# Performance work log

Hardware: AMD Instinct MI355X
Metric: run time of the kernel (lower is better)

## Reference

```python
import jax, jax.numpy as jnp
import numpy as np

DIM = 768
NUM_HEADS = 12
HEAD_DIM = 64  # attn_head_dim override
ALL_HEAD_DIM = NUM_HEADS * HEAD_DIM  # 768
SCALE = HEAD_DIM ** -0.5


def setup_inputs() -> dict:
    key = jax.random.key(0)
    ks = jax.random.split(key, 6)
    B, N = 8, 1024
    x = jax.random.normal(ks[0], (B, N, DIM), dtype=jnp.float32)
    w_qkv = jax.random.normal(ks[1], (3 * ALL_HEAD_DIM, DIM), dtype=jnp.float32) * (DIM ** -0.5)
    q_bias = jnp.zeros((ALL_HEAD_DIM,), dtype=jnp.float32)
    v_bias = jnp.zeros((ALL_HEAD_DIM,), dtype=jnp.float32)
    w_proj = jax.random.normal(ks[2], (DIM, ALL_HEAD_DIM), dtype=jnp.float32) * (ALL_HEAD_DIM ** -0.5)
    b_proj = jnp.zeros((DIM,), dtype=jnp.float32)
    return {"x": x, "w_qkv": w_qkv, "q_bias": q_bias, "v_bias": v_bias,
            "w_proj": w_proj, "b_proj": b_proj}


def reference(x, w_qkv, q_bias, v_bias, w_proj, b_proj):
    B, N, C = x.shape
    # qkv bias: [q_bias, zeros (k has no bias), v_bias]
    qkv_bias = jnp.concatenate([q_bias, jnp.zeros_like(v_bias), v_bias])
    qkv = x @ w_qkv.T + qkv_bias                      # [B, N, 3*ALL_HEAD_DIM]
    qkv = qkv.reshape(B, N, 3, NUM_HEADS, HEAD_DIM).transpose(2, 0, 3, 1, 4)
    q, k, v = qkv[0], qkv[1], qkv[2]                  # each [B, H, N, D]
    attn = jnp.einsum('bhqd,bhkd->bhqk', q * SCALE, k)
    attn = jax.nn.softmax(attn, axis=-1)
    out = jnp.einsum('bhqk,bhkd->bhqd', attn, v)      # [B, H, N, D]
    out = out.transpose(0, 2, 1, 3).reshape(B, N, ALL_HEAD_DIM)
    out = out @ w_proj.T + b_proj                     # [B, N, C]
    return out
```

## Files before the change

kernel.cpp:

```cpp
#include <hip/hip_runtime.h>
#include <hip/hip_bf16.h>

typedef unsigned short u16;
typedef unsigned int u32;
typedef __attribute__((ext_vector_type(4))) float f32x4;
typedef __attribute__((ext_vector_type(16))) float f32x16;
typedef __attribute__((ext_vector_type(8))) short bf16x8;

__device__ inline u16 f2bf(float f) {
    union { float f; u32 u; } v; v.f = f;
    u32 r = v.u + 0x7fff + ((v.u >> 16) & 1);
    return (u16)(r >> 16);
}

__device__ inline f32x4 mfma16(bf16x8 a, bf16x8 b, f32x4 c) {
    return __builtin_amdgcn_mfma_f32_16x16x32_bf16(a, b, c, 0, 0, 0);
}
__device__ inline f32x16 mfma32(bf16x8 a, bf16x8 b, f32x16 c) {
    return __builtin_amdgcn_mfma_f32_32x32x16_bf16(a, b, c, 0, 0, 0);
}
__device__ inline u32 cvtpk(float lo, float hi) {
    u32 r;
    asm("v_cvt_pk_bf16_f32 %0, %1, %2" : "=v"(r) : "v"(lo), "v"(hi));
    return r;
}
__device__ inline float exp2v(float x) {
    float r;
    asm("v_exp_f32 %0, %1" : "=v"(r) : "v"(x));
    return r;
}

__device__ inline void gload_lds16(const void* g, const void* l) {
    __builtin_amdgcn_global_load_lds(
        (const __attribute__((address_space(1))) void*)g,
        (__attribute__((address_space(3))) void*)l, 16, 0, 0);
}

#define QSCALE 0.18033688f

__global__ void cvt_kernel(const float* __restrict__ in, u16* __restrict__ out, int n8) {
    int i = blockIdx.x * 256 + threadIdx.x;
    if (i >= n8) return;
    const float4* p = (const float4*)in;
    float4 a = p[2 * i], b = p[2 * i + 1];
    bf16x8 v;
    v[0] = (short)f2bf(a.x); v[1] = (short)f2bf(a.y);
    v[2] = (short)f2bf(a.z); v[3] = (short)f2bf(a.w);
    v[4] = (short)f2bf(b.x); v[5] = (short)f2bf(b.y);
    v[6] = (short)f2bf(b.z); v[7] = (short)f2bf(b.w);
    ((bf16x8*)out)[i] = v;
}

template <int EPI>
__global__ __launch_bounds__(256) void gemm_bt(
    const u16* __restrict__ A, const u16* __restrict__ B,
    int M, int N, int K,
    u16* __restrict__ qw, u16* __restrict__ kw, u16* __restrict__ vw,
    const float* __restrict__ qb, const float* __restrict__ vb,
    float* __restrict__ outp, const float* __restrict__ bproj)
{
    __shared__ __align__(16) u16 lA[2][128 * 32];
    __shared__ __align__(16) u16 lB[2][128 * 32];
    const int tid = threadIdx.x;
    const int lane = tid & 63;
    const int wv = tid >> 6;
    const int nbn = N >> 7;
    const int bm = blockIdx.x / nbn, bn = blockIdx.x % nbn;
    const int row0 = bm << 7, col0 = bn << 7;

    const int c0 = tid, c1 = tid + 256;
    const int ldsOff0 = (wv * 64) * 8;
    const int ldsOff1 = (256 + wv * 64) * 8;

    f32x4 acc[4][4];
#pragma unroll
    for (int i = 0; i < 4; i++)
#pragma unroll
        for (int j = 0; j < 4; j++) acc[i][j] = (f32x4){0.f, 0.f, 0.f, 0.f};

    const int nT = K >> 5;

    auto stage = [&](int buf, int t) {
        const int k0 = t << 5;
        gload_lds16(&A[(size_t)(row0 + (c0 >> 2)) * K + k0 + (c0 & 3) * 8], &lA[buf][ldsOff0]);
        gload_lds16(&A[(size_t)(row0 + (c1 >> 2)) * K + k0 + (c1 & 3) * 8], &lA[buf][ldsOff1]);
        gload_lds16(&B[(size_t)(col0 + (c0 >> 2)) * K + k0 + (c0 & 3) * 8], &lB[buf][ldsOff0]);
        gload_lds16(&B[(size_t)(col0 + (c1 >> 2)) * K + k0 + (c1 & 3) * 8], &lB[buf][ldsOff1]);
    };

    const int wr = (wv >> 1) << 6;
    const int wc = (wv & 1) << 6;

    stage(0, 0);
    __syncthreads();
    for (int t = 0; t < nT; ++t) {
        if (t + 1 < nT) stage((t + 1) & 1, t + 1);
        const int buf = t & 1;
        const u16* As = &lA[buf][(wr + (lane & 15)) * 32 + ((lane >> 4) * 8)];
        const u16* Bs = &lB[buf][(wc + (lane & 15)) * 32 + ((lane >> 4) * 8)];
        bf16x8 af[4], bfr[4];
#pragma unroll
        for (int i = 0; i < 4; i++) af[i] = *(const bf16x8*)(As + i * 16 * 32);
#pragma unroll
        for (int i = 0; i < 4; i++) bfr[i] = *(const bf16x8*)(Bs + i * 16 * 32);
#pragma unroll
        for (int i = 0; i < 4; i++)
#pragma unroll
            for (int j = 0; j < 4; j++)
                acc[i][j] = mfma16(af[i], bfr[j], acc[i][j]);
        __syncthreads();
    }

    if (EPI == 0) {
#pragma unroll
        for (int nj = 0; nj < 4; ++nj) {
            const int col = col0 + wc + nj * 16 + (lane & 15);
            const int part = col / 768;
            const int rem = col - part * 768;
            const int h = rem >> 6, d = rem & 63;
            if (part == 2) {
                const float bias = vb[rem];
                const int fbase = ((d >> 5) << 1);
                const int dl = d & 31;
#pragma unroll
                for (int mi = 0; mi < 4; ++mi) {
                    const int rowb = row0 + wr + mi * 16 + ((lane >> 4) << 2);
                    const int bb = rowb >> 10, nb = rowb & 1023;
                    const int t2 = nb >> 5, kin = nb & 31;
                    const int f = fbase + (kin >> 4);
                    const int lane_ = (((kin >> 3) & 1) << 5) + dl;
                    ushort4 pk;
                    pk.x = f2bf(acc[mi][nj][0] + bias);
                    pk.y = f2bf(acc[mi][nj][1] + bias);
                    pk.z = f2bf(acc[mi][nj][2] + bias);
                    pk.w = f2bf(acc[mi][nj][3] + bias);
                    *(ushort4*)&vw[((size_t)(bb * 12 + h) << 16) + (t2 << 11) +
                                   (f << 9) + (lane_ << 3) + (nb & 7)] = pk;
                }
            } else if (part == 1) {
                const int joff = (d >> 3) << 8, e = d & 7;
#pragma unroll
                for (int mi = 0; mi < 4; ++mi) {
#pragma unroll
                    for (int j = 0; j < 4; ++j) {
                        const int row = row0 + wr + mi * 16 + ((lane >> 4) << 2) + j;
                        const int bb = row >> 10, n = row & 1023;
                        kw[((size_t)(bb * 12 + h) << 16) + ((n >> 5) << 11) + joff +
                           ((n & 31) << 3) + e] = f2bf(acc[mi][nj][j]);
                    }
                }
            } else {
                const float bias = qb[rem];
#pragma unroll
                for (int mi = 0; mi < 4; ++mi) {
#pragma unroll
                    for (int j = 0; j < 4; ++j) {
                        const int row = row0 + wr + mi * 16 + ((lane >> 4) << 2) + j;
                        const int bb = row >> 10, n = row & 1023;
                        qw[(size_t)(((bb * 12 + h) << 10) + n) * 64 + d] =
                            f2bf((acc[mi][nj][j] + bias) * QSCALE);
                    }
                }
            }
        }
    } else {
#pragma unroll
        for (int nj = 0; nj < 4; ++nj) {
            const int col = col0 + wc + nj * 16 + (lane & 15);
            const float bias = bproj[col];
#pragma unroll
            for (int mi = 0; mi < 4; ++mi) {
#pragma unroll
                for (int j = 0; j < 4; ++j) {
                    const int row = row0 + wr + mi * 16 + ((lane >> 4) << 2) + j;
                    outp[(size_t)row * N + col] = acc[mi][nj][j] + bias;
                }
            }
        }
    }
}

__global__ __launch_bounds__(256, 3) void attn_fwd(
    const u16* __restrict__ Q, const u16* __restrict__ KF,
    const u16* __restrict__ VF, u16* __restrict__ O)
{
    __shared__ __align__(16) u16 tlds[4][32 * 68];
    const int tid = threadIdx.x, lane = tid & 63, wv = tid >> 6;
    const int l31 = lane & 31, hi = lane >> 5;
    const int bh = blockIdx.x % 96;
    const int qbk = blockIdx.x / 96;
    const int q0 = qbk * 128 + wv * 32;
    const size_t base = (size_t)bh << 16;
    const u16* Qp = Q + base;
    const u16* Kp = KF + base;
    const u16* Vp = VF + base;

    bf16x8 qf0, qf1, qf2, qf3;
    {
        const u16* qrow = &Qp[(q0 + l31) * 64 + hi * 8];
        qf0 = *(const bf16x8*)(qrow);
        qf1 = *(const bf16x8*)(qrow + 16);
        qf2 = *(const bf16x8*)(qrow + 32);
        qf3 = *(const bf16x8*)(qrow + 48);
    }

    f32x16 ot0, ot1;
#pragma unroll
    for (int i = 0; i < 16; ++i) { ot0[i] = 0.f; ot1[i] = 0.f; }
    float m = -1e30f, l = 0.f;

    auto loadK = [&](int t2048, bf16x8& f0, bf16x8& f1, bf16x8& f2, bf16x8& f3) {
        const u16* kr = &Kp[t2048 + hi * 256 + l31 * 8];
        f0 = *(const bf16x8*)(kr);
        f1 = *(const bf16x8*)(kr + 512);
        f2 = *(const bf16x8*)(kr + 1024);
        f3 = *(const bf16x8*)(kr + 1536);
    };

    auto body = [&](int t2048, bf16x8 k0, bf16x8 k1, bf16x8 k2, bf16x8 k3) {
        f32x16 s;
#pragma unroll
        for (int i = 0; i < 16; ++i) s[i] = 0.f;
        __builtin_amdgcn_s_setprio(1);
        s = mfma32(k0, qf0, s);
        s = mfma32(k1, qf1, s);
        s = mfma32(k2, qf2, s);
        s = mfma32(k3, qf3, s);
        __builtin_amdgcn_s_setprio(0);
        const u16* vrow = &Vp[t2048 + lane * 8];
        bf16x8 vf00 = *(const bf16x8*)(vrow);
        bf16x8 vf01 = *(const bf16x8*)(vrow + 512);
        bf16x8 vf10 = *(const bf16x8*)(vrow + 1024);
        bf16x8 vf11 = *(const bf16x8*)(vrow + 1536);
        float t0 = fmaxf(fmaxf(s[0], s[1]), fmaxf(s[2], s[3]));
        float t1 = fmaxf(fmaxf(s[4], s[5]), fmaxf(s[6], s[7]));
        float t2 = fmaxf(fmaxf(s[8], s[9]), fmaxf(s[10], s[11]));
        float t3 = fmaxf(fmaxf(s[12], s[13]), fmaxf(s[14], s[15]));
        float tmax = fmaxf(fmaxf(t0, t1), fmaxf(t2, t3));
        tmax = fmaxf(tmax, __shfl_xor(tmax, 32));
        if (!__all(tmax - m <= 8.f)) {
            const float nm = fmaxf(m, tmax);
            const float cr = exp2v(m - nm);
#pragma unroll
            for (int i = 0; i < 16; ++i) { ot0[i] *= cr; ot1[i] *= cr; }
            l *= cr; m = nm;
        }
#pragma unroll
        for (int i = 0; i < 16; ++i) { float p = exp2v(s[i] - m); s[i] = p; l += p; }
        u32 w0 = cvtpk(s[0],  s[1]),  w1 = cvtpk(s[2],  s[3]);
        u32 w2 = cvtpk(s[4],  s[5]),  w3 = cvtpk(s[6],  s[7]);
        u32 w4 = cvtpk(s[8],  s[9]),  w5 = cvtpk(s[10], s[11]);
        u32 w6 = cvtpk(s[12], s[13]), w7 = cvtpk(s[14], s[15]);
        asm("v_permlane32_swap_b32 %0, %1" : "+v"(w0), "+v"(w2));
        asm("v_permlane32_swap_b32 %0, %1" : "+v"(w1), "+v"(w3));
        asm("v_permlane32_swap_b32 %0, %1" : "+v"(w4), "+v"(w6));
        asm("v_permlane32_swap_b32 %0, %1" : "+v"(w5), "+v"(w7));
        union { u32 u[4]; bf16x8 v; } pb0, pb1;
        pb0.u[0] = w0; pb0.u[1] = w1; pb0.u[2] = w2; pb0.u[3] = w3;
        pb1.u[0] = w4; pb1.u[1] = w5; pb1.u[2] = w6; pb1.u[3] = w7;
        __builtin_amdgcn_s_setprio(1);
        ot0 = mfma32(vf00, pb0.v, ot0);
        ot0 = mfma32(vf01, pb1.v, ot0);
        ot1 = mfma32(vf10, pb0.v, ot1);
        ot1 = mfma32(vf11, pb1.v, ot1);
        __builtin_amdgcn_s_setprio(0);
    };

    bf16x8 ka0, ka1, ka2, ka3, kb0, kb1, kb2, kb3;
    loadK(0, ka0, ka1, ka2, ka3);
    for (int kt = 0; kt < 32; kt += 2) {
        loadK((kt + 1) << 11, kb0, kb1, kb2, kb3);
        body(kt << 11, ka0, ka1, ka2, ka3);
        if (kt + 2 < 32) loadK((kt + 2) << 11, ka0, ka1, ka2, ka3);
        body((kt + 1) << 11, kb0, kb1, kb2, kb3);
    }

    const float lt = l + __shfl_xor(l, 32);
    const float inv = 1.f / lt;
    u16* tw = &tlds[wv][0];
    u32* tw32 = (u32*)tw;
#pragma unroll
    for (int i = 0; i < 8; ++i) {
        const int dl = 2 * (i & 1) + 8 * (i >> 1) + 4 * hi;
        tw32[(l31 * 68 + dl) >> 1]      = cvtpk(ot0[2 * i] * inv, ot0[2 * i + 1] * inv);
        tw32[(l31 * 68 + dl + 32) >> 1] = cvtpk(ot1[2 * i] * inv, ot1[2 * i + 1] * inv);
    }
    __syncthreads();
    const int b = bh / 12, h = bh - b * 12;
    const size_t obase = ((size_t)(b << 10) + q0) * 768 + h * 64 + (lane & 7) * 8;
#pragma unroll
    for (int it = 0; it < 4; ++it) {
        const int r = it * 8 + (lane >> 3);
        bf16x8 v = *(const bf16x8*)&tw[r * 68 + (lane & 7) * 8];
        *(bf16x8*)&O[obase + (size_t)r * 768] = v;
    }
}

extern "C" void kernel_launch(void* const* d_in, const int* in_sizes, int n_in,
                              void* d_out, int out_size, void* d_ws, size_t ws_size,
                              hipStream_t stream) {
    const float* x      = (const float*)d_in[0];
    const float* w_qkv  = (const float*)d_in[1];
    const float* q_bias = (const float*)d_in[2];
    const float* v_bias = (const float*)d_in[3];
    const float* w_proj = (const float*)d_in[4];
    const float* b_proj = (const float*)d_in[5];
    float* out = (float*)d_out;

    char* ws = (char*)d_ws;
    u16* xb     = (u16*)(ws);
    u16* wqkvb  = (u16*)(ws + 12582912);
    u16* wprojb = (u16*)(ws + 16121856);
    u16* qw     = (u16*)(ws + 17301504);
    u16* kw     = (u16*)(ws + 29884416);
    u16* vt     = (u16*)(ws + 42467328);
    u16* ob     = (u16*)(ws + 55050240);

    cvt_kernel<<<786432 / 256, 256, 0, stream>>>(x, xb, 786432);
    cvt_kernel<<<221184 / 256, 256, 0, stream>>>(w_qkv, wqkvb, 221184);
    cvt_kernel<<< 73728 / 256, 256, 0, stream>>>(w_proj, wprojb, 73728);

    gemm_bt<0><<<(8192 / 128) * (2304 / 128), 256, 0, stream>>>(
        xb, wqkvb, 8192, 2304, 768, qw, kw, vt, q_bias, v_bias, nullptr, nullptr);

    attn_fwd<<<96 * 8, 256, 0, stream>>>(qw, kw, vt, ob);

    gemm_bt<1><<<(8192 / 128) * (768 / 128), 256, 0, stream>>>(
        ob, wprojb, 8192, 768, 768, nullptr, nullptr, nullptr, nullptr, nullptr, out, b_proj);
}
```

Baseline: 129.3 us.

## Stage QKV GEMM epilogue through swizzled LDS for vectorized global stores

Rewrites the QKV GEMM epilogue so each tile's results are first written to a swizzled shared-memory buffer (reusing the staging buffers), then copied out with 16-byte vector stores into the Q, K and V layouts. This replaces the scattered 2-byte scalar stores used for Q and K. Also remaps block indices in groups of 8 to improve L2 locality, and issues the next prefetch after computing LDS pointers. The cost is an extra barrier and an LDS round trip per tile.

```diff
diff --git a/kernel.cpp b/kernel.cpp
--- a/kernel.cpp
+++ b/kernel.cpp
@@ -59,13 +59,19 @@
     const float* __restrict__ qb, const float* __restrict__ vb,
     float* __restrict__ outp, const float* __restrict__ bproj)
 {
-    __shared__ __align__(16) u16 lA[2][128 * 32];
-    __shared__ __align__(16) u16 lB[2][128 * 32];
+    __shared__ __align__(16) u16 smem[16384];
+    u16* lA0 = smem;
+    u16* lA1 = smem + 4096;
+    u16* lB0 = smem + 8192;
+    u16* lB1 = smem + 12288;
+
     const int tid = threadIdx.x;
     const int lane = tid & 63;
     const int wv = tid >> 6;
     const int nbn = N >> 7;
-    const int bm = blockIdx.x / nbn, bn = blockIdx.x % nbn;
+    const int nwg = gridDim.x;
+    const int wg = (blockIdx.x & 7) * (nwg >> 3) + (blockIdx.x >> 3);
+    const int bm = wg / nbn, bn = wg % nbn;
     const int row0 = bm << 7, col0 = bn << 7;
 
     const int c0 = tid, c1 = tid + 256;
@@ -80,24 +86,24 @@
 
     const int nT = K >> 5;
 
-    auto stage = [&](int buf, int t) {
+    auto stage = [&](u16* bufA, u16* bufB, int t) {
         const int k0 = t << 5;
-        gload_lds16(&A[(size_t)(row0 + (c0 >> 2)) * K + k0 + (c0 & 3) * 8], &lA[buf][ldsOff0]);
-        gload_lds16(&A[(size_t)(row0 + (c1 >> 2)) * K + k0 + (c1 & 3) * 8], &lA[buf][ldsOff1]);
-        gload_lds16(&B[(size_t)(col0 + (c0 >> 2)) * K + k0 + (c0 & 3) * 8], &lB[buf][ldsOff0]);
-        gload_lds16(&B[(size_t)(col0 + (c1 >> 2)) * K + k0 + (c1 & 3) * 8], &lB[buf][ldsOff1]);
+        gload_lds16(&A[(size_t)(row0 + (c0 >> 2)) * K + k0 + (c0 & 3) * 8], bufA + ldsOff0);
+        gload_lds16(&A[(size_t)(row0 + (c1 >> 2)) * K + k0 + (c1 & 3) * 8], bufA + ldsOff1);
+        gload_lds16(&B[(size_t)(col0 + (c0 >> 2)) * K + k0 + (c0 & 3) * 8], bufB + ldsOff0);
+        gload_lds16(&B[(size_t)(col0 + (c1 >> 2)) * K + k0 + (c1 & 3) * 8], bufB + ldsOff1);
     };
 
     const int wr = (wv >> 1) << 6;
     const int wc = (wv & 1) << 6;
 
-    stage(0, 0);
+    stage(lA0, lB0, 0);
     __syncthreads();
     for (int t = 0; t < nT; ++t) {
-        if (t + 1 < nT) stage((t + 1) & 1, t + 1);
-        const int buf = t & 1;
-        const u16* As = &lA[buf][(wr + (lane & 15)) * 32 + ((lane >> 4) * 8)];
-        const u16* Bs = &lB[buf][(wc + (lane & 15)) * 32 + ((lane >> 4) * 8)];
+        const u16* As = ((t & 1) ? lA1 : lA0) + (wr + (lane & 15)) * 32 + ((lane >> 4) * 8);
+        const u16* Bs = ((t & 1) ? lB1 : lB0) + (wc + (lane & 15)) * 32 + ((lane >> 4) * 8);
+        if (t + 1 < nT)
+            stage((t & 1) ? lA0 : lA1, (t & 1) ? lB0 : lB1, t + 1);
         bf16x8 af[4], bfr[4];
 #pragma unroll
         for (int i = 0; i < 4; i++) af[i] = *(const bf16x8*)(As + i * 16 * 32);
@@ -112,55 +118,78 @@
     }
 
     if (EPI == 0) {
-#pragma unroll
-        for (int nj = 0; nj < 4; ++nj) {
-            const int col = col0 + wc + nj * 16 + (lane & 15);
-            const int part = col / 768;
-            const int rem = col - part * 768;
-            const int h = rem >> 6, d = rem & 63;
-            if (part == 2) {
-                const float bias = vb[rem];
-                const int fbase = ((d >> 5) << 1);
-                const int dl = d & 31;
+        const int part = col0 / 768;
+        const int colr0 = col0 - part * 768;
+        const int h0 = colr0 >> 6;
+        const int bb = row0 >> 10;
+        const int n0 = row0 & 1023;
+
+        if (part < 2) {
+#pragma unroll
+            for (int nj = 0; nj < 4; ++nj) {
+                const int col = wc + nj * 16 + (lane & 15);
+                const float bias = (part == 0) ? qb[colr0 + col] : 0.f;
+                const float sc = (part == 0) ? QSCALE : 1.f;
 #pragma unroll
                 for (int mi = 0; mi < 4; ++mi) {
-                    const int rowb = row0 + wr + mi * 16 + ((lane >> 4) << 2);
-                    const int bb = rowb >> 10, nb = rowb & 1023;
-                    const int t2 = nb >> 5, kin = nb & 31;
-                    const int f = fbase + (kin >> 4);
-                    const int lane_ = (((kin >> 3) & 1) << 5) + dl;
+#pragma unroll
+                    for (int j = 0; j < 4; ++j) {
+                        const int row = wr + mi * 16 + ((lane >> 4) << 2) + j;
+                        smem[row * 128 + ((((col >> 3) ^ (row & 7)) << 3) | (col & 7))] =
+                            f2bf((acc[mi][nj][j] + bias) * sc);
+                    }
+                }
+            }
+        } else {
+#pragma unroll
+            for (int nj = 0; nj < 4; ++nj) {
+                const int col = wc + nj * 16 + (lane & 15);
+                const float bias = vb[colr0 + col];
+#pragma unroll
+                for (int mi = 0; mi < 4; ++mi) {
+                    const int row = wr + mi * 16 + ((lane >> 4) << 2);
                     ushort4 pk;
                     pk.x = f2bf(acc[mi][nj][0] + bias);
                     pk.y = f2bf(acc[mi][nj][1] + bias);
                     pk.z = f2bf(acc[mi][nj][2] + bias);
                     pk.w = f2bf(acc[mi][nj][3] + bias);
-                    *(ushort4*)&vw[((size_t)(bb * 12 + h) << 16) + (t2 << 11) +
-                                   (f << 9) + (lane_ << 3) + (nb & 7)] = pk;
+                    *(ushort4*)&smem[col * 128 +
+                        ((((row >> 3) ^ (col & 7)) << 3) | (row & 7))] = pk;
                 }
-            } else if (part == 1) {
-                const int joff = (d >> 3) << 8, e = d & 7;
-#pragma unroll
-                for (int mi = 0; mi < 4; ++mi) {
-#pragma unroll
-                    for (int j = 0; j < 4; ++j) {
-                        const int row = row0 + wr + mi * 16 + ((lane >> 4) << 2) + j;
-                        const int bb = row >> 10, n = row & 1023;
-                        kw[((size_t)(bb * 12 + h) << 16) + ((n >> 5) << 11) + joff +
-                           ((n & 31) << 3) + e] = f2bf(acc[mi][nj][j]);
-                    }
-                }
-            } else {
-                const float bias = qb[rem];
-#pragma unroll
-                for (int mi = 0; mi < 4; ++mi) {
-#pragma unroll
-                    for (int j = 0; j < 4; ++j) {
-                        const int row = row0 + wr + mi * 16 + ((lane >> 4) << 2) + j;
-                        const int bb = row >> 10, n = row & 1023;
-                        qw[(size_t)(((bb * 12 + h) << 10) + n) * 64 + d] =
-                            f2bf((acc[mi][nj][j] + bias) * QSCALE);
-                    }
-                }
+            }
+        }
+        __syncthreads();
+
+        if (part == 0) {
+#pragma unroll
+            for (int p = 0; p < 8; ++p) {
+                const int c = p * 256 + tid;
+                const int h = c >> 10, ri = (c >> 3) & 127, j = c & 7;
+                bf16x8 v = *(const bf16x8*)&smem[ri * 128 + (((h * 8 + j) ^ (ri & 7)) << 3)];
+                *(bf16x8*)&qw[((size_t)(((bb * 12 + h0 + h) << 10) + n0 + ri)) * 64 + j * 8] = v;
+            }
+        } else if (part == 1) {
+#pragma unroll
+            for (int p = 0; p < 8; ++p) {
+                const int c = p * 256 + tid;
+                const int h = c >> 10, t2 = (c >> 8) & 3, j = (c >> 5) & 7, r = c & 31;
+                const int ri = t2 * 32 + r;
+                bf16x8 v = *(const bf16x8*)&smem[ri * 128 + (((h * 8 + j) ^ (ri & 7)) << 3)];
+                *(bf16x8*)&kw[((size_t)(bb * 12 + h0 + h) << 16) +
+                              (((n0 >> 5) + t2) << 11) + (j << 8) + (r << 3)] = v;
+            }
+        } else {
+#pragma unroll
+            for (int p = 0; p < 8; ++p) {
+                const int c = p * 256 + tid;
+                const int h = c >> 10, w = c & 1023;
+                const int t2 = w >> 8, f = (w >> 6) & 3, ln = w & 63;
+                const int d = ((f >> 1) << 5) + (ln & 31);
+                const int rb = t2 * 32 + ((f & 1) << 4) + ((ln >> 5) << 3);
+                const int ct = h * 64 + d;
+                bf16x8 v = *(const bf16x8*)&smem[ct * 128 + (((rb >> 3) ^ (ct & 7)) << 3)];
+                *(bf16x8*)&vw[((size_t)(bb * 12 + h0 + h) << 16) +
+                              (((n0 >> 5) + t2) << 11) + (f << 9) + (ln << 3)] = v;
             }
         }
     } else {
```

After: 123.3 us. 4.6% less time.
